# Optimization experiments

Measured on AMD Instinct MI355X. Metric: run time of the kernel, lower is better.

Reference implementation:

```python
import jax, jax.numpy as jnp
import numpy as np

B, PS, H, W = 32, 1536, 32, 64
TNS = H * W                 # total_num_selects = 2048
NJ = TNS // 16              # num_joints = 128
QK = PS // 4                # q/k channels = 384
NC = 200                    # num_classes
BN_EPS = 1e-5


def setup_inputs() -> dict:
    key = jax.random.key(0)
    ks = jax.random.split(key, 8)
    s = 0.02  # small init scale for weights
    inp = {
        "x": jax.random.normal(ks[0], (B, PS, H, W), jnp.float32),
        # param_pool0: Linear(TNS -> NJ)
        "w_pool0": jax.random.normal(ks[1], (NJ, TNS), jnp.float32) * s,
        "b_pool0": jnp.zeros((NJ,), jnp.float32),
        # learnable adjacency: eye/100 + 1/100
        "adj1": jnp.eye(NJ, dtype=jnp.float32) / 100.0 + 1.0 / 100.0,
        # conv_q1 / conv_k1: Conv1d(PS -> PS//4, kernel=1)
        "w_q": jax.random.normal(ks[2], (QK, PS), jnp.float32) * s,
        "b_q": jnp.zeros((QK,), jnp.float32),
        "w_k": jax.random.normal(ks[3], (QK, PS), jnp.float32) * s,
        "b_k": jnp.zeros((QK,), jnp.float32),
        # alpha1 (torch inits to 0; we use 0.1 so attention branch has nonzero effect/grads)
        "alpha": jnp.array([0.1], jnp.float32),
        # conv1: Conv1d(PS -> PS, kernel=1)
        "w_c1": jax.random.normal(ks[4], (PS, PS), jnp.float32) * s,
        "b_c1": jnp.zeros((PS,), jnp.float32),
        # batch_norm1 affine params
        "gamma": jnp.ones((PS,), jnp.float32),
        "beta": jnp.zeros((PS,), jnp.float32),
        # param_pool1: Linear(NJ -> 1)
        "w_pool1": jax.random.normal(ks[5], (1, NJ), jnp.float32) * s,
        "b_pool1": jnp.zeros((1,), jnp.float32),
        # classifier: Linear(PS -> NC)
        "w_cls": jax.random.normal(ks[6], (NC, PS), jnp.float32) * s,
        "b_cls": jnp.zeros((NC,), jnp.float32),
    }
    return inp


def reference(x, w_pool0, b_pool0, adj1, w_q, b_q, w_k, b_k, alpha,
              w_c1, b_c1, gamma, beta, w_pool1, b_pool1, w_cls, b_cls):
    b, c = x.shape[0], x.shape[1]
    hs = x.reshape(b, c, -1)                                   # (B, PS, TNS)
    # param_pool0: pool selects down to joints
    hs = jnp.einsum('bcs,js->bcj', hs, w_pool0) + b_pool0      # (B, PS, NJ)
    # 1x1-conv q/k then mean over channel dim
    q1 = (jnp.einsum('oc,bcj->boj', w_q, hs) + b_q[:, None]).mean(axis=1)  # (B, NJ)
    k1 = (jnp.einsum('oc,bcj->boj', w_k, hs) + b_k[:, None]).mean(axis=1)  # (B, NJ)
    # outer-difference attention, tanh-bounded, blended with learnable adjacency
    A1 = adj1 + jnp.tanh(q1[:, :, None] - k1[:, None, :]) * alpha[0]       # (B, NJ, NJ)
    # conv1 (1x1) then adjacency-weighted matmul
    hs = jnp.einsum('oc,bcj->boj', w_c1, hs) + b_c1[:, None]   # (B, PS, NJ)
    hs = jnp.einsum('bcj,bjk->bck', hs, A1)                    # (B, PS, NJ)
    # BatchNorm1d over (batch, joints) per channel (training-mode batch stats)
    mean = hs.mean(axis=(0, 2))
    var = hs.var(axis=(0, 2))
    hs = (hs - mean[None, :, None]) * jax.lax.rsqrt(var + BN_EPS)[None, :, None]
    hs = gamma[None, :, None] * hs + beta[None, :, None]
    # param_pool1 (NJ -> 1), dropout is identity in eval, flatten, classify
    hs = jnp.einsum('bcj,j->bc', hs, w_pool1[0]) + b_pool1[0]  # (B, PS)
    out = hs @ w_cls.T + b_cls                                 # (B, NC)
    return out
```

## Files before the change

kernel.cpp:

```cpp
#include <hip/hip_runtime.h>
#include <hip/hip_bf16.h>

#define B_ 32
#define PS_ 1536
#define TNS_ 2048
#define NJ_ 128
#define QK_ 384
#define NC_ 200
#define BN_EPS_ 1e-5f

typedef __attribute__((ext_vector_type(8))) short short8;
typedef __attribute__((ext_vector_type(4))) float float4v;
typedef unsigned short ushort_t;

__device__ __forceinline__ unsigned short f2b(float f) {
    unsigned int u = __float_as_uint(f);
    return (unsigned short)((u + 0x7FFFu + ((u >> 16) & 1u)) >> 16);
}
__device__ __forceinline__ float b2f_lo(unsigned int u) { return __uint_as_float(u << 16); }
__device__ __forceinline__ float b2f_hi(unsigned int u) { return __uint_as_float(u & 0xffff0000u); }

__device__ __forceinline__ void mma_chunk(const short* As, const short* Bs,
                                          int wm, int wn, int lane, float4v acc[4][4]) {
    const int m0 = wm + (lane & 15);
    const int n0 = wn + (lane & 15);
    const int quad = lane >> 4;
    #pragma unroll
    for (int kk = 0; kk < 64; kk += 32) {
        short8 a[4], b[4];
        const int kb = quad * 8 + kk;
        #pragma unroll
        for (int i = 0; i < 4; ++i) {
            a[i] = *(const short8*)&As[(m0 + i * 16) * 72 + kb];
            b[i] = *(const short8*)&Bs[(n0 + i * 16) * 72 + kb];
        }
        #pragma unroll
        for (int i = 0; i < 4; ++i)
            #pragma unroll
            for (int j = 0; j < 4; ++j)
                acc[i][j] = __builtin_amdgcn_mfma_f32_16x16x32_bf16(a[i], b[j], acc[i][j], 0, 0, 0);
    }
}

__device__ __forceinline__ void stage_f32(const float* __restrict__ src, size_t stride,
                                          short* dst, int tid) {
    #pragma unroll
    for (int p = 0; p < 8; ++p) {
        int r = (tid >> 4) + p * 16;
        int kq = (tid & 15) * 4;
        float4 v = *(const float4*)(src + (size_t)r * stride + kq);
        ushort4 u = { f2b(v.x), f2b(v.y), f2b(v.z), f2b(v.w) };
        *(ushort4*)&dst[r * 72 + kq] = u;
    }
}
__device__ __forceinline__ void stage_b16(const ushort_t* __restrict__ src, size_t stride,
                                          short* dst, int tid) {
    #pragma unroll
    for (int p = 0; p < 4; ++p) {
        int r = (tid >> 3) + p * 32;
        int kq = (tid & 7) * 8;
        uint4 v = *(const uint4*)(src + (size_t)r * stride + kq);
        *(uint4*)&dst[r * 72 + kq] = v;
    }
}

__global__ void k_prep(const float* __restrict__ wq, const float* __restrict__ bq,
                       const float* __restrict__ wk, const float* __restrict__ bk,
                       const float* __restrict__ wp1,
                       float* __restrict__ wqb, float* __restrict__ wkb,
                       float* __restrict__ scal) {
    const int blk = blockIdx.x;
    const int tid = threadIdx.x;
    if (blk < 6) {
        int c = blk * 256 + tid;
        float s = 0.f;
        for (int o = 0; o < QK_; ++o) s += wq[(size_t)o * PS_ + c];
        wqb[c] = s * (1.0f / QK_);
    } else if (blk < 12) {
        int c = (blk - 6) * 256 + tid;
        float s = 0.f;
        for (int o = 0; o < QK_; ++o) s += wk[(size_t)o * PS_ + c];
        wkb[c] = s * (1.0f / QK_);
    } else {
        __shared__ float red[256];
        float s = (tid < QK_ ? bq[tid] : 0.f) + (tid + 256 < QK_ ? bq[tid + 256] : 0.f);
        red[tid] = s; __syncthreads();
        for (int off = 128; off > 0; off >>= 1) { if (tid < off) red[tid] += red[tid + off]; __syncthreads(); }
        if (tid == 0) scal[0] = red[0] * (1.0f / QK_);
        __syncthreads();
        s = (tid < QK_ ? bk[tid] : 0.f) + (tid + 256 < QK_ ? bk[tid + 256] : 0.f);
        red[tid] = s; __syncthreads();
        for (int off = 128; off > 0; off >>= 1) { if (tid < off) red[tid] += red[tid + off]; __syncthreads(); }
        if (tid == 0) scal[1] = red[0] * (1.0f / QK_);
        __syncthreads();
        s = (tid < NJ_ ? wp1[tid] : 0.f);
        red[tid] = s; __syncthreads();
        for (int off = 128; off > 0; off >>= 1) { if (tid < off) red[tid] += red[tid + off]; __syncthreads(); }
        if (tid == 0) scal[2] = red[0];
    }
}

__global__ void k_f2b4(const float* __restrict__ src, ushort_t* __restrict__ dst, int n4) {
    int i = blockIdx.x * 256 + threadIdx.x;
    if (i < n4) {
        float4 v = ((const float4*)src)[i];
        ushort4 u = { f2b(v.x), f2b(v.y), f2b(v.z), f2b(v.w) };
        ((ushort4*)dst)[i] = u;
    }
}

__global__ __launch_bounds__(256) void k_gemm1(const float* __restrict__ x,
        const ushort_t* __restrict__ w0b, const float* __restrict__ b0,
        ushort_t* __restrict__ hsT) {
    __shared__ __align__(16) short As[128 * 72];
    __shared__ __align__(16) short Bs[128 * 72];
    const int tid = threadIdx.x, lane = tid & 63, wave = tid >> 6;
    const int wm = (wave >> 1) * 64, wn = (wave & 1) * 64;
    const size_t m0 = (size_t)blockIdx.x * 128;
    float4v acc[4][4] = {};
    for (int k0 = 0; k0 < TNS_; k0 += 64) {
        stage_f32(x + m0 * TNS_ + k0, TNS_, As, tid);
        stage_b16(w0b + k0, TNS_, Bs, tid);
        __syncthreads();
        mma_chunk(As, Bs, wm, wn, lane, acc);
        __syncthreads();
    }
    const int b = blockIdx.x / 12, cb = (blockIdx.x % 12) * 128;
    const int quad = lane >> 4;
    #pragma unroll
    for (int jn = 0; jn < 4; ++jn) {
        int j = wn + jn * 16 + (lane & 15);
        float bj = b0[j];
        #pragma unroll
        for (int im = 0; im < 4; ++im) {
            int c = cb + wm + im * 16 + quad * 4;
            float4v v = acc[im][jn];
            ushort4 u = { f2b(v[0] + bj), f2b(v[1] + bj), f2b(v[2] + bj), f2b(v[3] + bj) };
            *(ushort4*)&hsT[((size_t)(b * NJ_ + j)) * PS_ + c] = u;
        }
    }
}

__global__ __launch_bounds__(256) void k_q1k1(const ushort_t* __restrict__ hsT,
        const float* __restrict__ wqb, const float* __restrict__ wkb,
        float* __restrict__ q1, float* __restrict__ k1) {
    int wid = blockIdx.x * 4 + (threadIdx.x >> 6);
    int lane = threadIdx.x & 63;
    int b = wid >> 7, j = wid & 127;
    const unsigned int* row = (const unsigned int*)(hsT + ((size_t)(b * NJ_ + j)) * PS_);
    float sq = 0.f, sk = 0.f;
    #pragma unroll
    for (int i = 0; i < 12; ++i) {
        unsigned int u = row[i * 64 + lane];
        int c = (i * 64 + lane) * 2;
        float v0 = b2f_lo(u), v1 = b2f_hi(u);
        sq += wqb[c] * v0 + wqb[c + 1] * v1;
        sk += wkb[c] * v0 + wkb[c + 1] * v1;
    }
    #pragma unroll
    for (int off = 32; off > 0; off >>= 1) { sq += __shfl_down(sq, off, 64); sk += __shfl_down(sk, off, 64); }
    if (lane == 0) { q1[b * NJ_ + j] = sq; k1[b * NJ_ + j] = sk; }
}

__global__ void k_a1(const float* __restrict__ adj, const float* __restrict__ q1,
                     const float* __restrict__ k1, const float* __restrict__ alpha,
                     const float* __restrict__ scal, ushort_t* __restrict__ A1t) {
    int idx = blockIdx.x * 256 + threadIdx.x;
    int b = idx >> 14;
    int r = idx & 16383;
    int j2 = r >> 7;
    int j = r & 127;
    float dbias = scal[0] - scal[1];
    float t = tanhf(q1[b * NJ_ + j] - k1[b * NJ_ + j2] + dbias);
    A1t[idx] = f2b(adj[j * NJ_ + j2] + t * alpha[0]);
}

__global__ __launch_bounds__(256) void k_gemm2(const ushort_t* __restrict__ wc1b,
        const float* __restrict__ bc1, const ushort_t* __restrict__ hsT,
        ushort_t* __restrict__ hs2) {
    __shared__ __align__(16) short As[128 * 72];
    __shared__ __align__(16) short Bs[128 * 72];
    const int tid = threadIdx.x, lane = tid & 63, wave = tid >> 6;
    const int wm = (wave >> 1) * 64, wn = (wave & 1) * 64;
    const int b = blockIdx.y, ob = blockIdx.x * 128;
    float4v acc[4][4] = {};
    const ushort_t* Abase = wc1b + (size_t)ob * PS_;
    const ushort_t* Bbase = hsT + (size_t)b * NJ_ * PS_;
    for (int k0 = 0; k0 < PS_; k0 += 64) {
        stage_b16(Abase + k0, PS_, As, tid);
        stage_b16(Bbase + k0, PS_, Bs, tid);
        __syncthreads();
        mma_chunk(As, Bs, wm, wn, lane, acc);
        __syncthreads();
    }
    const int quad = lane >> 4;
    #pragma unroll
    for (int im = 0; im < 4; ++im) {
        int o0 = ob + wm + im * 16 + quad * 4;
        float bc[4] = { bc1[o0], bc1[o0 + 1], bc1[o0 + 2], bc1[o0 + 3] };
        #pragma unroll
        for (int jn = 0; jn < 4; ++jn) {
            int j = wn + jn * 16 + (lane & 15);
            float4v v = acc[im][jn];
            #pragma unroll
            for (int r = 0; r < 4; ++r)
                hs2[((size_t)(b * PS_) + o0 + r) * NJ_ + j] = f2b(v[r] + bc[r]);
        }
    }
}

__global__ __launch_bounds__(256) void k_gemm3(const ushort_t* __restrict__ hs2,
        const ushort_t* __restrict__ A1t, ushort_t* __restrict__ hs3b) {
    __shared__ __align__(16) short As[128 * 72];
    __shared__ __align__(16) short Bs[128 * 72];
    const int tid = threadIdx.x, lane = tid & 63, wave = tid >> 6;
    const int wm = (wave >> 1) * 64, wn = (wave & 1) * 64;
    const int b = blockIdx.y, cbs = blockIdx.x * 128;
    float4v acc[4][4] = {};
    const ushort_t* Abase = hs2 + ((size_t)(b * PS_) + cbs) * NJ_;
    const ushort_t* Bbase = A1t + (size_t)b * NJ_ * NJ_;
    for (int k0 = 0; k0 < NJ_; k0 += 64) {
        stage_b16(Abase + k0, NJ_, As, tid);
        stage_b16(Bbase + k0, NJ_, Bs, tid);
        __syncthreads();
        mma_chunk(As, Bs, wm, wn, lane, acc);
        __syncthreads();
    }
    const int quad = lane >> 4;
    #pragma unroll
    for (int im = 0; im < 4; ++im) {
        int c0 = cbs + wm + im * 16 + quad * 4;
        #pragma unroll
        for (int jn = 0; jn < 4; ++jn) {
            int j2 = wn + jn * 16 + (lane & 15);
            float4v v = acc[im][jn];
            #pragma unroll
            for (int r = 0; r < 4; ++r)
                hs3b[((size_t)(b * PS_) + c0 + r) * NJ_ + j2] = f2b(v[r]);
        }
    }
}

__global__ void k_bnstats(const ushort_t* __restrict__ hs3b,
                          float* __restrict__ bnsum, float* __restrict__ bnsq) {
    int c = blockIdx.x, tid = threadIdx.x;
    float s = 0.f, q = 0.f;
    for (int b = 0; b < B_; ++b) {
        float v = __uint_as_float(((unsigned int)hs3b[((size_t)(b * PS_) + c) * NJ_ + tid]) << 16);
        s += v; q += v * v;
    }
    __shared__ float ss[2], qq[2];
    #pragma unroll
    for (int off = 32; off > 0; off >>= 1) { s += __shfl_down(s, off, 64); q += __shfl_down(q, off, 64); }
    int w = tid >> 6;
    if ((tid & 63) == 0) { ss[w] = s; qq[w] = q; }
    __syncthreads();
    if (tid == 0) { bnsum[c] = ss[0] + ss[1]; bnsq[c] = qq[0] + qq[1]; }
}

__global__ void k_pool(const ushort_t* __restrict__ hs3b, const float* __restrict__ bnsum,
                       const float* __restrict__ bnsq, const float* __restrict__ gamma,
                       const float* __restrict__ beta, const float* __restrict__ wp1,
                       const float* __restrict__ bp1, const float* __restrict__ scal,
                       float* __restrict__ p) {
    int gid = blockIdx.x * 256 + threadIdx.x;
    int row = gid >> 6;
    int lane = gid & 63;
    int c = row % PS_;
    const unsigned int* hp = (const unsigned int*)(hs3b + (size_t)row * NJ_);
    unsigned int u = hp[lane];
    float d = wp1[2 * lane] * b2f_lo(u) + wp1[2 * lane + 1] * b2f_hi(u);
    #pragma unroll
    for (int off = 32; off > 0; off >>= 1) d += __shfl_down(d, off, 64);
    if (lane == 0) {
        float mean = bnsum[c] * (1.0f / 4096.0f);
        float var = bnsq[c] * (1.0f / 4096.0f) - mean * mean;
        float s = gamma[c] * rsqrtf(var + BN_EPS_);
        p[row] = s * d + (beta[c] - s * mean) * scal[2] + bp1[0];
    }
}

__global__ void k_cls(const float* __restrict__ p, const float* __restrict__ wcls,
                      const float* __restrict__ bcls, float* __restrict__ out) {
    int gid = blockIdx.x * 256 + threadIdx.x;
    int w = gid >> 6;
    int lane = gid & 63;
    int b = w / 200, n = w % 200;
    const float* pp = p + (size_t)b * PS_;
    const float* wp = wcls + (size_t)n * PS_;
    float s = 0.f;
    for (int c = lane; c < PS_; c += 64) s += pp[c] * wp[c];
    #pragma unroll
    for (int off = 32; off > 0; off >>= 1) s += __shfl_down(s, off, 64);
    if (lane == 0) out[w] = s + bcls[n];
}

extern "C" void kernel_launch(void* const* d_in, const int* in_sizes, int n_in,
                              void* d_out, int out_size, void* d_ws, size_t ws_size,
                              hipStream_t stream) {
    const float* x       = (const float*)d_in[0];
    const float* w_pool0 = (const float*)d_in[1];
    const float* b_pool0 = (const float*)d_in[2];
    const float* adj1    = (const float*)d_in[3];
    const float* w_q     = (const float*)d_in[4];
    const float* b_q     = (const float*)d_in[5];
    const float* w_k     = (const float*)d_in[6];
    const float* b_k     = (const float*)d_in[7];
    const float* alpha   = (const float*)d_in[8];
    const float* w_c1    = (const float*)d_in[9];
    const float* b_c1    = (const float*)d_in[10];
    const float* gamma   = (const float*)d_in[11];
    const float* beta    = (const float*)d_in[12];
    const float* w_pool1 = (const float*)d_in[13];
    const float* b_pool1 = (const float*)d_in[14];
    const float* w_cls   = (const float*)d_in[15];
    const float* b_cls   = (const float*)d_in[16];
    float* out = (float*)d_out;

    ushort_t* hsT  = (ushort_t*)d_ws;
    ushort_t* hs2  = hsT + 6291456;
    ushort_t* hs3b = hs2 + 6291456;
    ushort_t* w0b  = hs3b + 6291456;
    ushort_t* wc1b = w0b + 262144;
    ushort_t* A1t  = wc1b + 2359296;
    float* fb    = (float*)(A1t + 524288);
    float* wqb   = fb;
    float* wkb   = wqb + 1536;
    float* scal  = wkb + 1536;
    float* q1    = scal + 16;
    float* k1    = q1 + 4096;
    float* bnsum = k1 + 4096;
    float* bnsq  = bnsum + 1536;
    float* pbuf  = bnsq + 1536;
    size_t need = 44040192u + (size_t)(1536 + 1536 + 16 + 4096 + 4096 + 1536 + 1536 + 49152) * 4;
    if (ws_size < need) return;

    k_prep <<<13, 256, 0, stream>>>(w_q, b_q, w_k, b_k, w_pool1, wqb, wkb, scal);
    k_f2b4 <<<256, 256, 0, stream>>>(w_pool0, w0b, 65536);
    k_f2b4 <<<2304, 256, 0, stream>>>(w_c1, wc1b, 589824);
    k_gemm1<<<384, 256, 0, stream>>>(x, w0b, b_pool0, hsT);
    k_q1k1 <<<1024, 256, 0, stream>>>(hsT, wqb, wkb, q1, k1);
    k_a1   <<<2048, 256, 0, stream>>>(adj1, q1, k1, alpha, scal, A1t);
    k_gemm2<<<dim3(12, 32), 256, 0, stream>>>(wc1b, b_c1, hsT, hs2);
    k_gemm3<<<dim3(12, 32), 256, 0, stream>>>(hs2, A1t, hs3b);
    k_bnstats<<<1536, 128, 0, stream>>>(hs3b, bnsum, bnsq);
    k_pool <<<12288, 256, 0, stream>>>(hs3b, bnsum, bnsq, gamma, beta, w_pool1, b_pool1, scal, pbuf);
    k_cls  <<<1600, 256, 0, stream>>>(pbuf, w_cls, b_cls, out);
}
```

Baseline: 686.7 us.

## Fuse conv1 and adjacency GEMMs with BN stats, add register-prefetch double buffering

Merges the weight-prep and bf16-conversion kernels into one launch. Fuses the conv1 GEMM, the adjacency GEMM and the batch-norm statistics into a single kernel: the intermediate tile stays in LDS and the column sums are reduced into global memory with atomics. It also adds register-prefetch double buffering to the main GEMM loops so global loads overlap with MFMA work. This removes the hs2 round trip, the separate stats pass and several launches, at the cost of more LDS per block, which may lower occupancy, and float atomics, which make the BN sums order-nondeterministic.

```diff
diff --git a/kernel.cpp b/kernel.cpp
--- a/kernel.cpp
+++ b/kernel.cpp
@@ -42,33 +42,50 @@
     }
 }
 
-__device__ __forceinline__ void stage_f32(const float* __restrict__ src, size_t stride,
-                                          short* dst, int tid) {
+__device__ __forceinline__ void load_f32(const float* __restrict__ src, size_t stride,
+                                         int tid, float4 r[8]) {
     #pragma unroll
     for (int p = 0; p < 8; ++p) {
-        int r = (tid >> 4) + p * 16;
+        int rr = (tid >> 4) + p * 16;
         int kq = (tid & 15) * 4;
-        float4 v = *(const float4*)(src + (size_t)r * stride + kq);
-        ushort4 u = { f2b(v.x), f2b(v.y), f2b(v.z), f2b(v.w) };
-        *(ushort4*)&dst[r * 72 + kq] = u;
-    }
-}
-__device__ __forceinline__ void stage_b16(const ushort_t* __restrict__ src, size_t stride,
-                                          short* dst, int tid) {
+        r[p] = *(const float4*)(src + (size_t)rr * stride + kq);
+    }
+}
+__device__ __forceinline__ void regs_to_lds_f32(short* dst, int tid, const float4 r[8]) {
+    #pragma unroll
+    for (int p = 0; p < 8; ++p) {
+        int rr = (tid >> 4) + p * 16;
+        int kq = (tid & 15) * 4;
+        ushort4 u = { f2b(r[p].x), f2b(r[p].y), f2b(r[p].z), f2b(r[p].w) };
+        *(ushort4*)&dst[rr * 72 + kq] = u;
+    }
+}
+__device__ __forceinline__ void load_b16(const ushort_t* __restrict__ src, size_t stride,
+                                         int tid, uint4 r[4]) {
     #pragma unroll
     for (int p = 0; p < 4; ++p) {
-        int r = (tid >> 3) + p * 32;
+        int rr = (tid >> 3) + p * 32;
         int kq = (tid & 7) * 8;
-        uint4 v = *(const uint4*)(src + (size_t)r * stride + kq);
-        *(uint4*)&dst[r * 72 + kq] = v;
-    }
-}
-
-__global__ void k_prep(const float* __restrict__ wq, const float* __restrict__ bq,
-                       const float* __restrict__ wk, const float* __restrict__ bk,
-                       const float* __restrict__ wp1,
-                       float* __restrict__ wqb, float* __restrict__ wkb,
-                       float* __restrict__ scal) {
+        r[p] = *(const uint4*)(src + (size_t)rr * stride + kq);
+    }
+}
+__device__ __forceinline__ void regs_to_lds_b16(short* dst, int tid, const uint4 r[4]) {
+    #pragma unroll
+    for (int p = 0; p < 4; ++p) {
+        int rr = (tid >> 3) + p * 32;
+        int kq = (tid & 7) * 8;
+        *(uint4*)&dst[rr * 72 + kq] = r[p];
+    }
+}
+
+__global__ void k_prep_all(const float* __restrict__ wq, const float* __restrict__ bq,
+                           const float* __restrict__ wk, const float* __restrict__ bk,
+                           const float* __restrict__ wp1,
+                           const float* __restrict__ w0, const float* __restrict__ wc1,
+                           float* __restrict__ wqb, float* __restrict__ wkb,
+                           float* __restrict__ scal,
+                           float* __restrict__ bnsum, float* __restrict__ bnsq,
+                           ushort_t* __restrict__ w0b, ushort_t* __restrict__ wc1b) {
     const int blk = blockIdx.x;
     const int tid = threadIdx.x;
     if (blk < 6) {
@@ -76,12 +93,13 @@
         float s = 0.f;
         for (int o = 0; o < QK_; ++o) s += wq[(size_t)o * PS_ + c];
         wqb[c] = s * (1.0f / QK_);
+        bnsum[c] = 0.f; bnsq[c] = 0.f;
     } else if (blk < 12) {
         int c = (blk - 6) * 256 + tid;
         float s = 0.f;
         for (int o = 0; o < QK_; ++o) s += wk[(size_t)o * PS_ + c];
         wkb[c] = s * (1.0f / QK_);
-    } else {
+    } else if (blk == 12) {
         __shared__ float red[256];
         float s = (tid < QK_ ? bq[tid] : 0.f) + (tid + 256 < QK_ ? bq[tid + 256] : 0.f);
         red[tid] = s; __syncthreads();
@@ -97,32 +115,49 @@
         red[tid] = s; __syncthreads();
         for (int off = 128; off > 0; off >>= 1) { if (tid < off) red[tid] += red[tid + off]; __syncthreads(); }
         if (tid == 0) scal[2] = red[0];
-    }
-}
-
-__global__ void k_f2b4(const float* __restrict__ src, ushort_t* __restrict__ dst, int n4) {
-    int i = blockIdx.x * 256 + threadIdx.x;
-    if (i < n4) {
-        float4 v = ((const float4*)src)[i];
+    } else if (blk < 269) {
+        int i = (blk - 13) * 256 + tid;
+        float4 v = ((const float4*)w0)[i];
         ushort4 u = { f2b(v.x), f2b(v.y), f2b(v.z), f2b(v.w) };
-        ((ushort4*)dst)[i] = u;
+        ((ushort4*)w0b)[i] = u;
+    } else {
+        int i = (blk - 269) * 256 + tid;
+        float4 v = ((const float4*)wc1)[i];
+        ushort4 u = { f2b(v.x), f2b(v.y), f2b(v.z), f2b(v.w) };
+        ((ushort4*)wc1b)[i] = u;
     }
 }
 
 __global__ __launch_bounds__(256) void k_gemm1(const float* __restrict__ x,
         const ushort_t* __restrict__ w0b, const float* __restrict__ b0,
         ushort_t* __restrict__ hsT) {
-    __shared__ __align__(16) short As[128 * 72];
-    __shared__ __align__(16) short Bs[128 * 72];
+    __shared__ __align__(16) short sm[4][128 * 72];
     const int tid = threadIdx.x, lane = tid & 63, wave = tid >> 6;
     const int wm = (wave >> 1) * 64, wn = (wave & 1) * 64;
     const size_t m0 = (size_t)blockIdx.x * 128;
     float4v acc[4][4] = {};
-    for (int k0 = 0; k0 < TNS_; k0 += 64) {
-        stage_f32(x + m0 * TNS_ + k0, TNS_, As, tid);
-        stage_b16(w0b + k0, TNS_, Bs, tid);
-        __syncthreads();
-        mma_chunk(As, Bs, wm, wn, lane, acc);
+    float4 ra[8]; uint4 rb[4];
+    load_f32(x + m0 * TNS_, TNS_, tid, ra);
+    load_b16(w0b, TNS_, tid, rb);
+    regs_to_lds_f32(sm[0], tid, ra);
+    regs_to_lds_b16(sm[1], tid, rb);
+    __syncthreads();
+    int cur = 0;
+    for (int k0 = 64; k0 <= TNS_; k0 += 64) {
+        const bool more = (k0 < TNS_);
+        if (more) {
+            load_f32(x + m0 * TNS_ + k0, TNS_, tid, ra);
+            load_b16(w0b + k0, TNS_, tid, rb);
+        }
+        __builtin_amdgcn_sched_barrier(0);
+        mma_chunk(sm[cur * 2], sm[cur * 2 + 1], wm, wn, lane, acc);
+        __builtin_amdgcn_sched_barrier(0);
+        if (more) {
+            int nx = cur ^ 1;
+            regs_to_lds_f32(sm[nx * 2], tid, ra);
+            regs_to_lds_b16(sm[nx * 2 + 1], tid, rb);
+            cur = nx;
+        }
         __syncthreads();
     }
     const int b = blockIdx.x / 12, cb = (blockIdx.x % 12) * 128;
@@ -175,87 +210,118 @@
     A1t[idx] = f2b(adj[j * NJ_ + j2] + t * alpha[0]);
 }
 
-__global__ __launch_bounds__(256) void k_gemm2(const ushort_t* __restrict__ wc1b,
+__global__ __launch_bounds__(256) void k_gemm23(const ushort_t* __restrict__ wc1b,
         const float* __restrict__ bc1, const ushort_t* __restrict__ hsT,
-        ushort_t* __restrict__ hs2) {
-    __shared__ __align__(16) short As[128 * 72];
-    __shared__ __align__(16) short Bs[128 * 72];
+        const ushort_t* __restrict__ A1t, ushort_t* __restrict__ hs3b,
+        float* __restrict__ bnsum, float* __restrict__ bnsq) {
+    __shared__ __align__(16) short sm[4][128 * 72];
+    __shared__ float bns_s[NJ_], bnq_s[NJ_];
     const int tid = threadIdx.x, lane = tid & 63, wave = tid >> 6;
     const int wm = (wave >> 1) * 64, wn = (wave & 1) * 64;
     const int b = blockIdx.y, ob = blockIdx.x * 128;
+    if (tid < NJ_) { bns_s[tid] = 0.f; bnq_s[tid] = 0.f; }
     float4v acc[4][4] = {};
     const ushort_t* Abase = wc1b + (size_t)ob * PS_;
     const ushort_t* Bbase = hsT + (size_t)b * NJ_ * PS_;
-    for (int k0 = 0; k0 < PS_; k0 += 64) {
-        stage_b16(Abase + k0, PS_, As, tid);
-        stage_b16(Bbase + k0, PS_, Bs, tid);
+    uint4 ra[4], rb[4];
+    load_b16(Abase, PS_, tid, ra);
+    load_b16(Bbase, PS_, tid, rb);
+    regs_to_lds_b16(sm[0], tid, ra);
+    regs_to_lds_b16(sm[1], tid, rb);
+    __syncthreads();
+    int cur = 0;
+    for (int k0 = 64; k0 <= PS_; k0 += 64) {
+        const bool more = (k0 < PS_);
+        if (more) {
+            load_b16(Abase + k0, PS_, tid, ra);
+            load_b16(Bbase + k0, PS_, tid, rb);
+        }
+        __builtin_amdgcn_sched_barrier(0);
+        mma_chunk(sm[cur * 2], sm[cur * 2 + 1], wm, wn, lane, acc);
+        __builtin_amdgcn_sched_barrier(0);
+        if (more) {
+            int nx = cur ^ 1;
+            regs_to_lds_b16(sm[nx * 2], tid, ra);
+            regs_to_lds_b16(sm[nx * 2 + 1], tid, rb);
+            cur = nx;
+        }
         __syncthreads();
-        mma_chunk(As, Bs, wm, wn, lane, acc);
-        __syncthreads();
-    }
+    }
+    short* C1 = &sm[0][0];
     const int quad = lane >> 4;
     #pragma unroll
     for (int im = 0; im < 4; ++im) {
-        int o0 = ob + wm + im * 16 + quad * 4;
-        float bc[4] = { bc1[o0], bc1[o0 + 1], bc1[o0 + 2], bc1[o0 + 3] };
+        int o0l = wm + im * 16 + quad * 4;
+        float bc[4] = { bc1[ob + o0l], bc1[ob + o0l + 1], bc1[ob + o0l + 2], bc1[ob + o0l + 3] };
         #pragma unroll
         for (int jn = 0; jn < 4; ++jn) {
             int j = wn + jn * 16 + (lane & 15);
             float4v v = acc[im][jn];
             #pragma unroll
             for (int r = 0; r < 4; ++r)
-                hs2[((size_t)(b * PS_) + o0 + r) * NJ_ + j] = f2b(v[r] + bc[r]);
-        }
-    }
-}
-
-__global__ __launch_bounds__(256) void k_gemm3(const ushort_t* __restrict__ hs2,
-        const ushort_t* __restrict__ A1t, ushort_t* __restrict__ hs3b) {
-    __shared__ __align__(16) short As[128 * 72];
-    __shared__ __align__(16) short Bs[128 * 72];
-    const int tid = threadIdx.x, lane = tid & 63, wave = tid >> 6;
-    const int wm = (wave >> 1) * 64, wn = (wave & 1) * 64;
-    const int b = blockIdx.y, cbs = blockIdx.x * 128;
-    float4v acc[4][4] = {};
-    const ushort_t* Abase = hs2 + ((size_t)(b * PS_) + cbs) * NJ_;
-    const ushort_t* Bbase = A1t + (size_t)b * NJ_ * NJ_;
-    for (int k0 = 0; k0 < NJ_; k0 += 64) {
-        stage_b16(Abase + k0, NJ_, As, tid);
-        stage_b16(Bbase + k0, NJ_, Bs, tid);
-        __syncthreads();
-        mma_chunk(As, Bs, wm, wn, lane, acc);
-        __syncthreads();
-    }
-    const int quad = lane >> 4;
+                C1[(o0l + r) * 136 + j] = (short)f2b(v[r] + bc[r]);
+        }
+    }
+    __syncthreads();
+    float4v acc2[4][4] = {};
+    const ushort_t* Ap = A1t + (size_t)b * NJ_ * NJ_;
+    const int m0 = wm + (lane & 15), n0 = wn + (lane & 15);
+    #pragma unroll
+    for (int kk = 0; kk < 128; kk += 32) {
+        short8 a[4], bf[4];
+        const int kb = quad * 8 + kk;
+        #pragma unroll
+        for (int i = 0; i < 4; ++i) a[i] = *(const short8*)&C1[(m0 + i * 16) * 136 + kb];
+        #pragma unroll
+        for (int j = 0; j < 4; ++j) bf[j] = *(const short8*)&Ap[(size_t)(n0 + j * 16) * NJ_ + kb];
+        #pragma unroll
+        for (int i = 0; i < 4; ++i)
+            #pragma unroll
+            for (int j = 0; j < 4; ++j)
+                acc2[i][j] = __builtin_amdgcn_mfma_f32_16x16x32_bf16(a[i], bf[j], acc2[i][j], 0, 0, 0);
+    }
+    float s_[4][4] = {}, q_[4][4] = {};
     #pragma unroll
     for (int im = 0; im < 4; ++im) {
-        int c0 = cbs + wm + im * 16 + quad * 4;
+        int c0l = wm + im * 16 + quad * 4;
         #pragma unroll
         for (int jn = 0; jn < 4; ++jn) {
             int j2 = wn + jn * 16 + (lane & 15);
-            float4v v = acc[im][jn];
-            #pragma unroll
-            for (int r = 0; r < 4; ++r)
-                hs3b[((size_t)(b * PS_) + c0 + r) * NJ_ + j2] = f2b(v[r]);
-        }
-    }
-}
-
-__global__ void k_bnstats(const ushort_t* __restrict__ hs3b,
-                          float* __restrict__ bnsum, float* __restrict__ bnsq) {
-    int c = blockIdx.x, tid = threadIdx.x;
-    float s = 0.f, q = 0.f;
-    for (int b = 0; b < B_; ++b) {
-        float v = __uint_as_float(((unsigned int)hs3b[((size_t)(b * PS_) + c) * NJ_ + tid]) << 16);
-        s += v; q += v * v;
-    }
-    __shared__ float ss[2], qq[2];
-    #pragma unroll
-    for (int off = 32; off > 0; off >>= 1) { s += __shfl_down(s, off, 64); q += __shfl_down(q, off, 64); }
-    int w = tid >> 6;
-    if ((tid & 63) == 0) { ss[w] = s; qq[w] = q; }
+            float4v v = acc2[im][jn];
+            #pragma unroll
+            for (int r = 0; r < 4; ++r) {
+                unsigned short us = f2b(v[r]);
+                float vr = b2f_lo((unsigned int)us);
+                s_[im][r] += vr; q_[im][r] += vr * vr;
+                hs3b[((size_t)(b * PS_) + ob + c0l + r) * NJ_ + j2] = us;
+            }
+        }
+    }
+    #pragma unroll
+    for (int m = 1; m < 16; m <<= 1) {
+        #pragma unroll
+        for (int im = 0; im < 4; ++im)
+            #pragma unroll
+            for (int r = 0; r < 4; ++r) {
+                s_[im][r] += __shfl_xor(s_[im][r], m, 64);
+                q_[im][r] += __shfl_xor(q_[im][r], m, 64);
+            }
+    }
+    if ((lane & 15) == 0) {
+        #pragma unroll
+        for (int im = 0; im < 4; ++im)
+            #pragma unroll
+            for (int r = 0; r < 4; ++r) {
+                int cl = wm + im * 16 + quad * 4 + r;
+                atomicAdd(&bns_s[cl], s_[im][r]);
+                atomicAdd(&bnq_s[cl], q_[im][r]);
+            }
+    }
     __syncthreads();
-    if (tid == 0) { bnsum[c] = ss[0] + ss[1]; bnsq[c] = qq[0] + qq[1]; }
+    if (tid < NJ_) {
+        atomicAdd(&bnsum[ob + tid], bns_s[tid]);
+        atomicAdd(&bnsq[ob + tid], bnq_s[tid]);
+    }
 }
 
 __global__ void k_pool(const ushort_t* __restrict__ hs3b, const float* __restrict__ bnsum,
@@ -335,15 +401,12 @@
     size_t need = 44040192u + (size_t)(1536 + 1536 + 16 + 4096 + 4096 + 1536 + 1536 + 49152) * 4;
     if (ws_size < need) return;
 
-    k_prep <<<13, 256, 0, stream>>>(w_q, b_q, w_k, b_k, w_pool1, wqb, wkb, scal);
-    k_f2b4 <<<256, 256, 0, stream>>>(w_pool0, w0b, 65536);
-    k_f2b4 <<<2304, 256, 0, stream>>>(w_c1, wc1b, 589824);
-    k_gemm1<<<384, 256, 0, stream>>>(x, w0b, b_pool0, hsT);
-    k_q1k1 <<<1024, 256, 0, stream>>>(hsT, wqb, wkb, q1, k1);
-    k_a1   <<<2048, 256, 0, stream>>>(adj1, q1, k1, alpha, scal, A1t);
-    k_gemm2<<<dim3(12, 32), 256, 0, stream>>>(wc1b, b_c1, hsT, hs2);
-    k_gemm3<<<dim3(12, 32), 256, 0, stream>>>(hs2, A1t, hs3b);
-    k_bnstats<<<1536, 128, 0, stream>>>(hs3b, bnsum, bnsq);
-    k_pool <<<12288, 256, 0, stream>>>(hs3b, bnsum, bnsq, gamma, beta, w_pool1, b_pool1, scal, pbuf);
-    k_cls  <<<1600, 256, 0, stream>>>(pbuf, w_cls, b_cls, out);
-}
+    k_prep_all<<<2573, 256, 0, stream>>>(w_q, b_q, w_k, b_k, w_pool1, w_pool0, w_c1,
+                                         wqb, wkb, scal, bnsum, bnsq, w0b, wc1b);
+    k_gemm1 <<<384, 256, 0, stream>>>(x, w0b, b_pool0, hsT);
+    k_q1k1  <<<1024, 256, 0, stream>>>(hsT, wqb, wkb, q1, k1);
+    k_a1    <<<2048, 256, 0, stream>>>(adj1, q1, k1, alpha, scal, A1t);
+    k_gemm23<<<dim3(12, 32), 256, 0, stream>>>(wc1b, b_c1, hsT, A1t, hs3b, bnsum, bnsq);
+    k_pool  <<<12288, 256, 0, stream>>>(hs3b, bnsum, bnsq, gamma, beta, w_pool1, b_pool1, scal, pbuf);
+    k_cls   <<<1600, 256, 0, stream>>>(pbuf, w_cls, b_cls, out);
+}
```

Result: slower. 771.1 us (+12.3%).
